# Optimization experiments

Hardware: AMD Instinct MI355X
Metric: run time of the kernel (lower is better)

## Reference

```python
import jax, jax.numpy as jnp
import numpy as np

B, S, H, OUT = 64, 513, 1024, 128   # batch, seq (incl CLS), hidden, slot labels
T = S - 1                            # subword tokens after dropping [CLS]
P_WORD_START = 0.75                  # avg ~1.33 subwords per word


def setup_inputs() -> dict:
    key = jax.random.key(0)
    k1, k2, k3, k4 = jax.random.split(key, 4)
    hidden_states = jax.random.normal(k1, (B, S, H), jnp.float32)
    W = jax.random.normal(k2, (H, OUT), jnp.float32) * 0.02
    b = jax.random.normal(k3, (OUT,), jnp.float32) * 0.02
    # contiguous, non-decreasing word ids: cumsum of word-start flags
    starts = (jax.random.uniform(k4, (B, T)) < P_WORD_START).astype(jnp.int32)
    starts = starts.at[:, 0].set(1)
    segment_ids = jnp.cumsum(starts, axis=-1) - 1  # [B, T], values in [0, n_words)
    return {"hidden_states": hidden_states, "W": W, "b": b,
            "segment_ids": segment_ids}


def _merge_row(logits, seg):
    # logits: [T, OUT], seg: [T] contiguous non-decreasing word ids
    s = jax.ops.segment_sum(logits, seg, num_segments=T)                    # [T, OUT]
    c = jax.ops.segment_sum(jnp.ones((T,), logits.dtype), seg, num_segments=T)
    mean = s / jnp.maximum(c, 1.0)[:, None]
    # words beyond n_words (empty segments) -> zero padding, as in the original
    return jnp.where(c[:, None] > 0, mean, 0.0)


def reference(hidden_states, W, b, segment_ids):
    x = hidden_states[:, 1:]                       # drop [CLS]; dropout = identity (eval)
    logits = jnp.einsum('bth,ho->bto', x, W) + b   # [B, T, OUT]
    merged = jax.vmap(_merge_row)(logits, segment_ids)  # per-word ragged mean + pad
    return jnp.transpose(merged, (0, 2, 1))        # [B, OUT, T]
```

## Files before the change

kernel.cpp:

```cpp
#include <hip/hip_runtime.h>
#include <hip/hip_bf16.h>

#define B_    64
#define S_    513
#define T_    512
#define H_    1024
#define OUT_  128
#define BK    32
#define NKT   (H_ / BK)
#define ROWS  96
#define OWN   64
#define LGS   132

typedef __attribute__((ext_vector_type(8))) short short8_t;
typedef __attribute__((ext_vector_type(4))) float f32x4;

__device__ inline ushort f2bf(float f) {
    union { float f; unsigned u; } x; x.f = f;
    unsigned r = x.u + 0x7fffu + ((x.u >> 16) & 1u);
    return (ushort)(r >> 16);
}
__device__ inline int4 pack8(const float4& a, const float4& b) {
    union { ushort u[8]; int4 v; } pk;
    pk.u[0] = f2bf(a.x); pk.u[1] = f2bf(a.y); pk.u[2] = f2bf(a.z); pk.u[3] = f2bf(a.w);
    pk.u[4] = f2bf(b.x); pk.u[5] = f2bf(b.y); pk.u[6] = f2bf(b.z); pk.u[7] = f2bf(b.w);
    return pk.v;
}

__global__ __launch_bounds__(256) void wt_kernel(
    const float* __restrict__ W, ushort* __restrict__ Wt)
{
    __shared__ ushort tile[64][65];
    int k0 = blockIdx.x * 64, o0 = blockIdx.y * 64;
    int tid = threadIdx.x;
#pragma unroll
    for (int p = 0; p < 16; ++p) {
        int idx = tid + p * 256;
        int r = idx >> 6, c = idx & 63;
        tile[r][c] = f2bf(W[(size_t)(k0 + r) * OUT_ + o0 + c]);
    }
    __syncthreads();
#pragma unroll
    for (int p = 0; p < 16; ++p) {
        int idx = tid + p * 256;
        int c = idx >> 6, r = idx & 63;
        Wt[(size_t)(o0 + c) * H_ + k0 + r] = tile[r][c];
    }
}

__global__ __launch_bounds__(256, 2) void fused_kernel(
    const float* __restrict__ hs, const ushort* __restrict__ Wt,
    const float* __restrict__ bias, const int* __restrict__ seg,
    float* __restrict__ out)
{
    union Smem {
        ushort As[2][ROWS * BK];
        float  lg[ROWS * LGS];
    };
    __shared__ Smem sm;
    __shared__ int sseg[ROWS];
    __shared__ int lstart[OWN];
    __shared__ int lcnt[OWN];
    __shared__ int sExt, sSlo;

    int bid  = blockIdx.x;
    int b    = bid >> 3;
    int tile = bid & 7;
    int t0   = tile * OWN;
    int Tl   = (T_ - t0) < ROWS ? (T_ - t0) : ROWS;

    int tid  = threadIdx.x;
    int lane = tid & 63;
    int w    = tid >> 6;
    int wm   = w & 1, wn = w >> 1;
    int l15  = lane & 15, ksl = lane >> 4;

    if (tid < Tl)  sseg[tid] = seg[b * T_ + t0 + tid];
    if (tid < OWN) { lstart[tid] = ROWS; lcnt[tid] = 0; }
    if (tid == 0)  sExt = Tl;
    __syncthreads();
    if (tid == 0) {
        int start0 = (t0 == 0) || (seg[b * T_ + t0 - 1] != sseg[0]);
        sSlo = sseg[0] + (start0 ? 0 : 1);
    }
    if (tid >= OWN && tid < Tl && sseg[tid] != sseg[tid - 1])
        atomicMin(&sExt, tid);
    __syncthreads();
    int ext  = sExt;
    int s_lo = sSlo;
    int s_hi = sseg[OWN - 1] + 1;
    if (tid < ext && sseg[tid] >= s_lo) {
        int li = sseg[tid] - s_lo;
        atomicMin(&lstart[li], tid);
        atomicAdd(&lcnt[li], 1);
    }

    int arow0 = tid >> 2;
    int ac    = tid & 3;
    int arow1 = 64 + arow0;
    const float* aptr0 = hs + ((size_t)(b * S_ + 1 + t0 + arow0)) * H_ + ac * 8;
    const float* aptr1 = hs + ((size_t)(b * S_ + 1 + t0 + arow1)) * H_ + ac * 8;
    bool doC1 = (tid < 128) && (arow1 < ext);
    int wA0 = arow0 * BK + ac * 8;
    int wA1 = arow1 * BK + ac * 8;

    const ushort* bp[4];
#pragma unroll
    for (int fn = 0; fn < 4; ++fn)
        bp[fn] = Wt + (size_t)(wn * 64 + fn * 16 + l15) * H_ + ksl * 8;

    f32x4 acc[3][4];
#pragma unroll
    for (int fm = 0; fm < 3; ++fm)
#pragma unroll
        for (int fn = 0; fn < 4; ++fn) acc[fm][fn] = (f32x4){0.f, 0.f, 0.f, 0.f};

    float4 ra0, ra1, ra2, ra3;
    short8_t bfA[4], bfB[4];

    auto loadA = [&](int kt) {
        const float* p = aptr0 + kt * BK;
        ra0 = *reinterpret_cast<const float4*>(p);
        ra1 = *reinterpret_cast<const float4*>(p + 4);
        if (doC1) {
            const float* q = aptr1 + kt * BK;
            ra2 = *reinterpret_cast<const float4*>(q);
            ra3 = *reinterpret_cast<const float4*>(q + 4);
        }
    };
    auto loadB = [&](short8_t* dst, int kt) {
#pragma unroll
        for (int fn = 0; fn < 4; ++fn)
            dst[fn] = *reinterpret_cast<const short8_t*>(bp[fn] + kt * BK);
    };
    auto writeA = [&](int nb) {
        *reinterpret_cast<int4*>(&sm.As[nb][wA0]) = pack8(ra0, ra1);
        if (doC1)
            *reinterpret_cast<int4*>(&sm.As[nb][wA1]) = pack8(ra2, ra3);
    };
    auto compute = [&](int cb, short8_t* bf) {
        short8_t af[3];
#pragma unroll
        for (int fm = 0; fm < 3; ++fm)
            af[fm] = *reinterpret_cast<const short8_t*>(
                &sm.As[cb][(wm * 48 + fm * 16 + l15) * BK + ksl * 8]);
#pragma unroll
        for (int fm = 0; fm < 3; ++fm)
#pragma unroll
            for (int fn = 0; fn < 4; ++fn)
                acc[fm][fn] = __builtin_amdgcn_mfma_f32_16x16x32_bf16(
                    af[fm], bf[fn], acc[fm][fn], 0, 0, 0);
    };

    loadB(bfA, 0); loadA(0);
    writeA(0);
    __syncthreads();

    for (int kt = 0; kt < NKT; kt += 2) {
        loadA(kt + 1); loadB(bfB, kt + 1);
        compute(0, bfA);
        writeA(1);
        __syncthreads();
        bool more = (kt + 2 < NKT);
        if (more) { loadA(kt + 2); loadB(bfA, kt + 2); }
        compute(1, bfB);
        if (more) writeA(0);
        __syncthreads();
    }

#pragma unroll
    for (int fm = 0; fm < 3; ++fm) {
        int rbase = wm * 48 + fm * 16 + ksl * 4;
#pragma unroll
        for (int fn = 0; fn < 4; ++fn) {
            int o = wn * 64 + fn * 16 + l15;
#pragma unroll
            for (int r = 0; r < 4; ++r)
                sm.lg[(rbase + r) * LGS + o] = acc[fm][fn][r];
        }
    }
    __syncthreads();

    int sl   = tid & 63;
    int ogrp = tid >> 6;
    int ns   = s_hi - s_lo;
    if (sl < ns) {
        int st = lstart[sl];
        int cn = lcnt[sl];
        float inv = 1.0f / (float)cn;
        float* dst = out + (size_t)b * OUT_ * T_ + s_lo + sl;
#pragma unroll 4
        for (int oi = 0; oi < 32; ++oi) {
            int o = ogrp + oi * 4;
            float sum = 0.f;
            for (int i = 0; i < cn; ++i) sum += sm.lg[(st + i) * LGS + o];
            dst[(size_t)o * T_] = sum * inv + bias[o];
        }
    }

    if (tile == 7) {
        for (int o = ogrp; o < OUT_; o += 4)
            for (int s = s_hi + sl; s < T_; s += 64)
                out[((size_t)b * OUT_ + o) * T_ + s] = 0.f;
    }
}

extern "C" void kernel_launch(void* const* d_in, const int* in_sizes, int n_in,
                              void* d_out, int out_size, void* d_ws, size_t ws_size,
                              hipStream_t stream) {
    const float* hs   = (const float*)d_in[0];
    const float* W    = (const float*)d_in[1];
    const float* bias = (const float*)d_in[2];
    const int*   seg  = (const int*)d_in[3];
    float* out = (float*)d_out;

    ushort* Wt = (ushort*)d_ws;

    wt_kernel<<<dim3(H_ / 64, OUT_ / 64), 256, 0, stream>>>(W, Wt);
    fused_kernel<<<B_ * (T_ / OWN), 256, 0, stream>>>(hs, Wt, bias, seg, out);
}
```

Before: 64.86 us.

## Load GEMM operands straight into registers, drop LDS staging, use 512 threads

Each wave now loads its own A fragments from global memory straight into registers and converts them with the packed v_cvt_pk_bf16_f32 instruction. This replaces the cooperative LDS double-buffer and the two barriers per k-step. The block grows to 512 threads, so each wave covers 32 output columns instead of 64, and the merge and zero-fill loops are re-strided to match. The aim is to remove LDS round-trips, synchronisation and software bf16 rounding. The cost is that the four column-waves re-read the same hidden-state rows, which relies on cache hits, and out-of-range rows are clamped to row 0 and loaded anyway.

```diff
diff --git a/kernel.cpp b/kernel.cpp
--- a/kernel.cpp
+++ b/kernel.cpp
@@ -6,10 +6,9 @@
 #define T_    512
 #define H_    1024
 #define OUT_  128
-#define BK    32
-#define NKT   (H_ / BK)
+#define NKT   32
+#define OWN   64
 #define ROWS  96
-#define OWN   64
 #define LGS   132
 
 typedef __attribute__((ext_vector_type(8))) short short8_t;
@@ -20,11 +19,14 @@
     unsigned r = x.u + 0x7fffu + ((x.u >> 16) & 1u);
     return (ushort)(r >> 16);
 }
-__device__ inline int4 pack8(const float4& a, const float4& b) {
-    union { ushort u[8]; int4 v; } pk;
-    pk.u[0] = f2bf(a.x); pk.u[1] = f2bf(a.y); pk.u[2] = f2bf(a.z); pk.u[3] = f2bf(a.w);
-    pk.u[4] = f2bf(b.x); pk.u[5] = f2bf(b.y); pk.u[6] = f2bf(b.z); pk.u[7] = f2bf(b.w);
-    return pk.v;
+
+__device__ inline short8_t cvt8(const float4& x, const float4& y) {
+    union { int i[4]; short8_t s; } u;
+    asm("v_cvt_pk_bf16_f32 %0, %1, %2" : "=v"(u.i[0]) : "v"(x.x), "v"(x.y));
+    asm("v_cvt_pk_bf16_f32 %0, %1, %2" : "=v"(u.i[1]) : "v"(x.z), "v"(x.w));
+    asm("v_cvt_pk_bf16_f32 %0, %1, %2" : "=v"(u.i[2]) : "v"(y.x), "v"(y.y));
+    asm("v_cvt_pk_bf16_f32 %0, %1, %2" : "=v"(u.i[3]) : "v"(y.z), "v"(y.w));
+    return u.s;
 }
 
 __global__ __launch_bounds__(256) void wt_kernel(
@@ -48,16 +50,12 @@
     }
 }
 
-__global__ __launch_bounds__(256, 2) void fused_kernel(
+__global__ __launch_bounds__(512, 4) void fused_kernel(
     const float* __restrict__ hs, const ushort* __restrict__ Wt,
     const float* __restrict__ bias, const int* __restrict__ seg,
     float* __restrict__ out)
 {
-    union Smem {
-        ushort As[2][ROWS * BK];
-        float  lg[ROWS * LGS];
-    };
-    __shared__ Smem sm;
+    __shared__ float lg[ROWS * LGS];
     __shared__ int sseg[ROWS];
     __shared__ int lstart[OWN];
     __shared__ int lcnt[OWN];
@@ -80,7 +78,7 @@
     if (tid == 0)  sExt = Tl;
     __syncthreads();
     if (tid == 0) {
-        int start0 = (t0 == 0) || (seg[b * T_ + t0 - 1] != sseg[0]);
+        bool start0 = (t0 == 0) || (seg[b * T_ + t0 - 1] != sseg[0]);
         sSlo = sseg[0] + (start0 ? 0 : 1);
     }
     if (tid >= OWN && tid < Tl && sseg[tid] != sseg[tid - 1])
@@ -89,94 +87,80 @@
     int ext  = sExt;
     int s_lo = sSlo;
     int s_hi = sseg[OWN - 1] + 1;
-    if (tid < ext && sseg[tid] >= s_lo) {
-        int li = sseg[tid] - s_lo;
-        atomicMin(&lstart[li], tid);
-        atomicAdd(&lcnt[li], 1);
-    }
-
-    int arow0 = tid >> 2;
-    int ac    = tid & 3;
-    int arow1 = 64 + arow0;
-    const float* aptr0 = hs + ((size_t)(b * S_ + 1 + t0 + arow0)) * H_ + ac * 8;
-    const float* aptr1 = hs + ((size_t)(b * S_ + 1 + t0 + arow1)) * H_ + ac * 8;
-    bool doC1 = (tid < 128) && (arow1 < ext);
-    int wA0 = arow0 * BK + ac * 8;
-    int wA1 = arow1 * BK + ac * 8;
-
-    const ushort* bp[4];
-#pragma unroll
-    for (int fn = 0; fn < 4; ++fn)
-        bp[fn] = Wt + (size_t)(wn * 64 + fn * 16 + l15) * H_ + ksl * 8;
-
-    f32x4 acc[3][4];
+    if (tid < ext) {
+        int sid = sseg[tid];
+        if (sid >= s_lo) {
+            atomicMin(&lstart[sid - s_lo], tid);
+            atomicAdd(&lcnt[sid - s_lo], 1);
+        }
+    }
+
+    const float* ap[3];
+#pragma unroll
+    for (int fm = 0; fm < 3; ++fm) {
+        int row = wm * 48 + fm * 16 + l15;
+        int re  = row < ext ? row : 0;
+        ap[fm] = hs + ((size_t)(b * S_ + 1 + t0 + re)) * H_ + ksl * 8;
+    }
+    const ushort* bp[2];
+#pragma unroll
+    for (int fn = 0; fn < 2; ++fn)
+        bp[fn] = Wt + (size_t)(wn * 32 + fn * 16 + l15) * H_ + ksl * 8;
+
+    f32x4 acc[3][2];
 #pragma unroll
     for (int fm = 0; fm < 3; ++fm)
 #pragma unroll
-        for (int fn = 0; fn < 4; ++fn) acc[fm][fn] = (f32x4){0.f, 0.f, 0.f, 0.f};
-
-    float4 ra0, ra1, ra2, ra3;
-    short8_t bfA[4], bfB[4];
-
-    auto loadA = [&](int kt) {
-        const float* p = aptr0 + kt * BK;
-        ra0 = *reinterpret_cast<const float4*>(p);
-        ra1 = *reinterpret_cast<const float4*>(p + 4);
-        if (doC1) {
-            const float* q = aptr1 + kt * BK;
-            ra2 = *reinterpret_cast<const float4*>(q);
-            ra3 = *reinterpret_cast<const float4*>(q + 4);
+        for (int fn = 0; fn < 2; ++fn) acc[fm][fn] = (f32x4){0.f, 0.f, 0.f, 0.f};
+
+    float4 xA[3][2], xB[3][2];
+    int4   yA[2],   yB[2];
+
+    auto LA = [&](float4 (&x)[3][2], int kt) {
+#pragma unroll
+        for (int fm = 0; fm < 3; ++fm) {
+            const float* p = ap[fm] + kt * 32;
+            x[fm][0] = *reinterpret_cast<const float4*>(p);
+            x[fm][1] = *reinterpret_cast<const float4*>(p + 4);
         }
     };
-    auto loadB = [&](short8_t* dst, int kt) {
-#pragma unroll
-        for (int fn = 0; fn < 4; ++fn)
-            dst[fn] = *reinterpret_cast<const short8_t*>(bp[fn] + kt * BK);
+    auto LB = [&](int4 (&y)[2], int kt) {
+#pragma unroll
+        for (int fn = 0; fn < 2; ++fn)
+            y[fn] = *reinterpret_cast<const int4*>(bp[fn] + kt * 32);
     };
-    auto writeA = [&](int nb) {
-        *reinterpret_cast<int4*>(&sm.As[nb][wA0]) = pack8(ra0, ra1);
-        if (doC1)
-            *reinterpret_cast<int4*>(&sm.As[nb][wA1]) = pack8(ra2, ra3);
-    };
-    auto compute = [&](int cb, short8_t* bf) {
-        short8_t af[3];
+    auto STEP = [&](float4 (&x)[3][2], int4 (&y)[2]) {
+        short8_t af[3], bf[2];
+#pragma unroll
+        for (int fm = 0; fm < 3; ++fm) af[fm] = cvt8(x[fm][0], x[fm][1]);
+#pragma unroll
+        for (int fn = 0; fn < 2; ++fn)
+            bf[fn] = *reinterpret_cast<short8_t*>(&y[fn]);
 #pragma unroll
         for (int fm = 0; fm < 3; ++fm)
-            af[fm] = *reinterpret_cast<const short8_t*>(
-                &sm.As[cb][(wm * 48 + fm * 16 + l15) * BK + ksl * 8]);
-#pragma unroll
-        for (int fm = 0; fm < 3; ++fm)
-#pragma unroll
-            for (int fn = 0; fn < 4; ++fn)
+#pragma unroll
+            for (int fn = 0; fn < 2; ++fn)
                 acc[fm][fn] = __builtin_amdgcn_mfma_f32_16x16x32_bf16(
                     af[fm], bf[fn], acc[fm][fn], 0, 0, 0);
     };
 
-    loadB(bfA, 0); loadA(0);
-    writeA(0);
-    __syncthreads();
-
+    LA(xA, 0); LB(yA, 0);
     for (int kt = 0; kt < NKT; kt += 2) {
-        loadA(kt + 1); loadB(bfB, kt + 1);
-        compute(0, bfA);
-        writeA(1);
-        __syncthreads();
-        bool more = (kt + 2 < NKT);
-        if (more) { loadA(kt + 2); loadB(bfA, kt + 2); }
-        compute(1, bfB);
-        if (more) writeA(0);
-        __syncthreads();
+        LA(xB, kt + 1); LB(yB, kt + 1);
+        STEP(xA, yA);
+        if (kt + 2 < NKT) { LA(xA, kt + 2); LB(yA, kt + 2); }
+        STEP(xB, yB);
     }
 
 #pragma unroll
     for (int fm = 0; fm < 3; ++fm) {
         int rbase = wm * 48 + fm * 16 + ksl * 4;
 #pragma unroll
-        for (int fn = 0; fn < 4; ++fn) {
-            int o = wn * 64 + fn * 16 + l15;
+        for (int fn = 0; fn < 2; ++fn) {
+            int o = wn * 32 + fn * 16 + l15;
 #pragma unroll
             for (int r = 0; r < 4; ++r)
-                sm.lg[(rbase + r) * LGS + o] = acc[fm][fn][r];
+                lg[(rbase + r) * LGS + o] = acc[fm][fn][r];
         }
     }
     __syncthreads();
@@ -190,16 +174,16 @@
         float inv = 1.0f / (float)cn;
         float* dst = out + (size_t)b * OUT_ * T_ + s_lo + sl;
 #pragma unroll 4
-        for (int oi = 0; oi < 32; ++oi) {
-            int o = ogrp + oi * 4;
+        for (int oi = 0; oi < 16; ++oi) {
+            int o = ogrp + oi * 8;
             float sum = 0.f;
-            for (int i = 0; i < cn; ++i) sum += sm.lg[(st + i) * LGS + o];
+            for (int i = 0; i < cn; ++i) sum += lg[(st + i) * LGS + o];
             dst[(size_t)o * T_] = sum * inv + bias[o];
         }
     }
 
     if (tile == 7) {
-        for (int o = ogrp; o < OUT_; o += 4)
+        for (int o = ogrp; o < OUT_; o += 8)
             for (int s = s_hi + sl; s < T_; s += 64)
                 out[((size_t)b * OUT_ + o) * T_ + s] = 0.f;
     }
@@ -217,5 +201,5 @@
     ushort* Wt = (ushort*)d_ws;
 
     wt_kernel<<<dim3(H_ / 64, OUT_ / 64), 256, 0, stream>>>(W, Wt);
-    fused_kernel<<<B_ * (T_ / OWN), 256, 0, stream>>>(hs, Wt, bias, seg, out);
-}
+    fused_kernel<<<B_ * (T_ / OWN), 512, 0, stream>>>(hs, Wt, bias, seg, out);
+}
```

New measurement: 112.3 us. +73.2%, slower.
